# Kernel tuning notes

Hardware: AMD Instinct MI355X
Metric: run time of the kernel (lower is better)

## Reference

```python
import jax, jax.numpy as jnp
import numpy as np

N = 100000        # nodes
E = 3200000       # edges (avg degree 32)
IN_F = 128
OUT_F = 64
ALPHA = 0.2       # LeakyReLU negative slope
EPS = 1e-5        # LayerNorm eps


def setup_inputs() -> dict:
    key = jax.random.key(0)
    k = jax.random.split(key, 5)
    x = jax.random.normal(k[0], (N, IN_F), jnp.float32)
    edge = jax.random.randint(k[1], (2, E), 0, N, dtype=jnp.int32)
    # kaiming-normal inits as in the torch module
    W = jax.random.normal(k[2], (OUT_F, IN_F), jnp.float32) * np.float32(np.sqrt(2.0 / IN_F))
    b = jnp.zeros((OUT_F,), jnp.float32)
    a = jax.random.normal(k[3], (2 * OUT_F,), jnp.float32) * np.float32(np.sqrt(2.0 / (2 * OUT_F)))
    gamma = jnp.ones((OUT_F,), jnp.float32)
    beta = jnp.zeros((OUT_F,), jnp.float32)
    return {"x": x, "edge": edge, "W": W, "b": b, "a": a, "gamma": gamma, "beta": beta}


def reference(x, edge, W, b, a, gamma, beta):
    # h = Linear(in->out)
    h = x @ W.T + b                                   # [N, OUT_F]
    src, dst = edge[0], edge[1]
    # edge score a · cat(h[src], h[dst]) == (h @ a_l)[src] + (h @ a_r)[dst]
    sl = h @ a[:OUT_F]                                # [N]
    sr = h @ a[OUT_F:]                                # [N]
    score = sl[src] + sr[dst]                         # [E]
    lrelu = jnp.where(score > 0, score, ALPHA * score)
    edge_e = jnp.exp(-lrelu)                          # [E] (dropout=0 / eval)
    # sparse spmm: h_prime[i] = sum_{e: src_e==i} edge_e * h[dst_e]
    msg = edge_e[:, None] * h[dst]                    # [E, OUT_F]
    h_prime = jax.ops.segment_sum(msg, src, num_segments=N)  # [N, OUT_F]
    # LayerNorm over feature dim (biased variance, as torch)
    mu = jnp.mean(h_prime, axis=-1, keepdims=True)
    var = jnp.mean(jnp.square(h_prime - mu), axis=-1, keepdims=True)
    h_norm = (h_prime - mu) * jax.lax.rsqrt(var + EPS) * gamma + beta
    # concat=True -> ELU
    return jax.nn.elu(h_norm)
```

## Files before the change

kernel.cpp:

```cpp
#include <hip/hip_runtime.h>
#include <hip/hip_fp16.h>
#include <cstdint>
#include <cstddef>

#define INF_  128
#define OUTF  64
#define ALPHA 0.2f
#define LN_EPS 1e-5f

#define PBLK2 256
#define BT2   512
#define TILE  8192
#define NP2   784
#define NPS   1024
#define PCAP2 48
#define LOC2  128
#define CSRCAP 4608

typedef __attribute__((ext_vector_type(8))) _Float16 half8;
typedef __attribute__((ext_vector_type(4))) float    f32x4;

__global__ __launch_bounds__(256) void gemm_kernel(
    const float* __restrict__ x, const float* __restrict__ W,
    const float* __restrict__ b, const float* __restrict__ a,
    __half* __restrict__ hh, float* __restrict__ sl, float* __restrict__ sr, int n)
{
    __shared__ half8 wfrag_lds[16][64];

    const int tid  = threadIdx.x;
    const int lane = tid & 63;
    const int wv   = tid >> 6;
    const int col  = lane & 15;
    const int quad = lane >> 4;

    for (int idx = tid; idx < 1024; idx += 256) {
        const int l  = idx & 63, ct = idx >> 6;
        const int c  = ct >> 2,  t  = ct & 3;
        const int row = 4 * (l & 15) + t;
        const int k0  = 32 * c + 8 * (l >> 4);
        const float4 f0 = ((const float4*)W)[row * 32 + (k0 >> 2)];
        const float4 f1 = ((const float4*)W)[row * 32 + (k0 >> 2) + 1];
        half8 h;
        h[0] = (_Float16)f0.x; h[1] = (_Float16)f0.y;
        h[2] = (_Float16)f0.z; h[3] = (_Float16)f0.w;
        h[4] = (_Float16)f1.x; h[5] = (_Float16)f1.y;
        h[6] = (_Float16)f1.z; h[7] = (_Float16)f1.w;
        wfrag_lds[ct][l] = h;
    }
    __syncthreads();

    half8 bf[4][4];
    #pragma unroll
    for (int c = 0; c < 4; c++)
        #pragma unroll
        for (int t = 0; t < 4; t++)
            bf[c][t] = wfrag_lds[c * 4 + t][lane];

    const float4 b4  = ((const float4*)b)[col];
    const float4 al4 = ((const float4*)a)[col];
    const float4 ar4 = ((const float4*)a)[16 + col];

    const int ntile  = (n + 15) >> 4;
    const int wgid   = blockIdx.x * 4 + wv;
    const int nwaves = gridDim.x * 4;

    for (int tile = wgid; tile < ntile; tile += nwaves) {
        const int node0 = tile << 4;
        const int xr    = min(node0 + col, n - 1);
        const float* xrow = x + (size_t)xr * INF_ + 8 * quad;

        f32x4 acc0 = {0,0,0,0}, acc1 = {0,0,0,0}, acc2 = {0,0,0,0}, acc3 = {0,0,0,0};
        #pragma unroll
        for (int c = 0; c < 4; c++) {
            const float4 f0 = *(const float4*)(xrow + 32 * c);
            const float4 f1 = *(const float4*)(xrow + 32 * c + 4);
            half8 af;
            af[0] = (_Float16)f0.x; af[1] = (_Float16)f0.y;
            af[2] = (_Float16)f0.z; af[3] = (_Float16)f0.w;
            af[4] = (_Float16)f1.x; af[5] = (_Float16)f1.y;
            af[6] = (_Float16)f1.z; af[7] = (_Float16)f1.w;
            acc0 = __builtin_amdgcn_mfma_f32_16x16x32_f16(af, bf[c][0], acc0, 0, 0, 0);
            acc1 = __builtin_amdgcn_mfma_f32_16x16x32_f16(af, bf[c][1], acc1, 0, 0, 0);
            acc2 = __builtin_amdgcn_mfma_f32_16x16x32_f16(af, bf[c][2], acc2, 0, 0, 0);
            acc3 = __builtin_amdgcn_mfma_f32_16x16x32_f16(af, bf[c][3], acc3, 0, 0, 0);
        }

        #pragma unroll
        for (int reg = 0; reg < 4; reg++) {
            const int node = node0 + quad * 4 + reg;
            const float v0 = acc0[reg] + b4.x;
            const float v1 = acc1[reg] + b4.y;
            const float v2 = acc2[reg] + b4.z;
            const float v3 = acc3[reg] + b4.w;
            float p = v0 * al4.x + v1 * al4.y + v2 * al4.z + v3 * al4.w;
            float q = v0 * ar4.x + v1 * ar4.y + v2 * ar4.z + v3 * ar4.w;
            p += __shfl_xor(p, 1); p += __shfl_xor(p, 2);
            p += __shfl_xor(p, 4); p += __shfl_xor(p, 8);
            q += __shfl_xor(q, 1); q += __shfl_xor(q, 2);
            q += __shfl_xor(q, 4); q += __shfl_xor(q, 8);
            if (node < n) {
                ushort4 u;
                u.x = __half_as_ushort(__float2half(v0));
                u.y = __half_as_ushort(__float2half(v1));
                u.z = __half_as_ushort(__float2half(v2));
                u.w = __half_as_ushort(__float2half(v3));
                ((ushort4*)hh)[(size_t)node * 16 + col] = u;
                if (col == 0) { sl[node] = p; sr[node] = q; }
            }
        }
    }
}

__global__ __launch_bounds__(512) void part_scatter(
    const int* __restrict__ src, const int* __restrict__ dst,
    int* __restrict__ pka, int* __restrict__ acnt, int E)
{
    __shared__ int hist[NPS];
    __shared__ int bnd[NPS + 1];
    __shared__ int cur[NPS];
    __shared__ int gbase[NP2];
    __shared__ int buf[TILE];
    __shared__ int csum[16];
    __shared__ int csb[16];

    const int t    = threadIdx.x;
    const int b    = blockIdx.x;
    const int lane = t & 63;
    const int wv   = t >> 6;

    for (int i = t; i < NP2; i += 512) gbase[i] = 0;

    const int chunk = (E + PBLK2 - 1) / PBLK2;
    const int lo = b * chunk;
    const int hi = min(E, lo + chunk);

    for (int tb = lo; tb < hi; tb += TILE) {
        const int tcnt = min(TILE, hi - tb);
        for (int i = t; i < NPS; i += 512) hist[i] = 0;
        __syncthreads();

        int pp[16], pay[16];
        #pragma unroll
        for (int k = 0; k < 16; k++) {
            const int e = tb + t + k * 512;
            pp[k] = -1;
            if (e < hi) {
                const int s = src[e];
                pp[k]  = s >> 7;
                pay[k] = ((s & 127) << 17) | dst[e];
                atomicAdd(&hist[pp[k]], 1);
            }
        }
        __syncthreads();

        int vA = hist[wv * 64 + lane];
        int vB = hist[(wv + 8) * 64 + lane];
        int sA = vA, sB = vB;
        #pragma unroll
        for (int d = 1; d < 64; d <<= 1) {
            const int uA = __shfl(sA, lane - d);
            const int uB = __shfl(sB, lane - d);
            if (lane >= d) { sA += uA; sB += uB; }
        }
        if (lane == 63) { csum[wv] = sA; csum[wv + 8] = sB; }
        __syncthreads();
        if (t == 0) {
            int r = 0;
            #pragma unroll
            for (int c2 = 0; c2 < 16; c2++) { csb[c2] = r; r += csum[c2]; }
            bnd[NPS] = r;
        }
        __syncthreads();
        {
            const int eA = csb[wv] + sA - vA;
            const int eB = csb[wv + 8] + sB - vB;
            bnd[wv * 64 + lane]       = eA;
            bnd[(wv + 8) * 64 + lane] = eB;
            cur[wv * 64 + lane]       = eA;
            cur[(wv + 8) * 64 + lane] = eB;
        }
        __syncthreads();

        #pragma unroll
        for (int k = 0; k < 16; k++) {
            if (pp[k] >= 0) {
                const int r = atomicAdd(&cur[pp[k]], 1);
                buf[r] = pay[k];
            }
        }
        __syncthreads();

        for (int idx = t; idx < tcnt; idx += 512) {
            int p = 0;
            #pragma unroll
            for (int step = 512; step >= 1; step >>= 1)
                if (bnd[p + step] <= idx) p += step;
            const int off = gbase[p] + (idx - bnd[p]);
            if (off < PCAP2)
                pka[(size_t)((p << 8) | b) * PCAP2 + off] = buf[idx];
        }
        __syncthreads();

        for (int p = t; p < NP2; p += 512) gbase[p] += bnd[p + 1] - bnd[p];
        __syncthreads();
    }

    for (int p = t; p < NP2; p += 512)
        acnt[p * PBLK2 + b] = min(gbase[p], PCAP2);
}

__global__ __launch_bounds__(512) void gat_fused(
    const int* __restrict__ pka, const int* __restrict__ acnt,
    const float* __restrict__ sl, const float* __restrict__ sr,
    const __half* __restrict__ hh,
    const float* __restrict__ gamma, const float* __restrict__ beta,
    float* __restrict__ out, int n)
{
    __shared__ int    ldst[CSRCAP];
    __shared__ __half lwgt[CSRCAP];
    __shared__ int    alen[PBLK2];
    __shared__ float  lsl[LOC2];
    __shared__ int    lhist[LOC2];
    __shared__ int    lbase[LOC2 + 1];
    __shared__ int    cur2[LOC2];
    __shared__ int    wtot_;

    const int B     = blockIdx.x;
    const int t     = threadIdx.x;
    const int lane  = t & 63;
    const int wv    = t >> 6;
    const int fgrp  = lane & 15;
    const int equad = lane >> 4;

    for (int i = t; i < PBLK2; i += 512) alen[i] = acnt[B * PBLK2 + i];
    if (t < LOC2) {
        lhist[t] = 0;
        const int g = (B << 7) + t;
        lsl[t] = (g < n) ? sl[g] : 0.f;
    }
    __syncthreads();

    const int4* slab4 = (const int4*)(pka + (size_t)(B << 8) * PCAP2);

    for (int i = t; i < 3072; i += 512) {
        const int j0  = i << 2;
        const int seg = j0 / PCAP2;
        const int off = j0 - seg * PCAP2;
        const int m   = alen[seg] - off;
        if (m > 0) {
            const int4 v4 = slab4[i];
            atomicAdd(&lhist[(v4.x >> 17) & 127], 1);
            if (m > 1) atomicAdd(&lhist[(v4.y >> 17) & 127], 1);
            if (m > 2) atomicAdd(&lhist[(v4.z >> 17) & 127], 1);
            if (m > 3) atomicAdd(&lhist[(v4.w >> 17) & 127], 1);
        }
    }
    __syncthreads();

    int sv = 0, vv = 0;
    if (t < 128) {
        vv = lhist[t]; sv = vv;
        #pragma unroll
        for (int d = 1; d < 64; d <<= 1) {
            const int u = __shfl(sv, lane - d);
            if (lane >= d) sv += u;
        }
        if (t == 63) wtot_ = sv;
    }
    __syncthreads();
    if (t < 128) {
        const int base = (t >= 64) ? wtot_ : 0;
        const int eb = base + sv - vv;
        lbase[t] = eb; cur2[t] = eb;
        if (t == 127) lbase[128] = base + sv;
    }
    __syncthreads();

    for (int i = t; i < 3072; i += 512) {
        const int j0  = i << 2;
        const int seg = j0 / PCAP2;
        const int off = j0 - seg * PCAP2;
        const int m   = alen[seg] - off;
        if (m > 0) {
            const int4 v4 = slab4[i];
            #pragma unroll
            for (int c = 0; c < 4; c++) {
                if (c < m) {
                    const int v = (c == 0) ? v4.x : (c == 1) ? v4.y : (c == 2) ? v4.z : v4.w;
                    const int s = (v >> 17) & 127;
                    const int d = v & 0x1FFFF;
                    const float sc = lsl[s] + sr[d];
                    const float lr = sc > 0.f ? sc : ALPHA * sc;
                    const int p = atomicAdd(&cur2[s], 1);
                    if (p < CSRCAP) {
                        ldst[p] = d;
                        lwgt[p] = __float2half(__expf(-lr));
                    }
                }
            }
        }
    }
    __syncthreads();

    const float4 gm4 = ((const float4*)gamma)[fgrp];
    const float4 bt4 = ((const float4*)beta)[fgrp];

    for (int k = wv; k < LOC2; k += 8) {
        const int node = (B << 7) + k;
        const int nb   = min(lbase[k], CSRCAP);
        const int ne   = min(lbase[k + 1], CSRCAP);
        const int len  = ne - nb;

        float4 acc = make_float4(0.f, 0.f, 0.f, 0.f);

        const int e0 = equad, e1 = 4 + equad;
        int dA = 0, dB = 0; float wA = 0.f, wB = 0.f;
        if (e0 < len) { dA = ldst[nb + e0]; wA = __half2float(lwgt[nb + e0]); }
        if (e1 < len) { dB = ldst[nb + e1]; wB = __half2float(lwgt[nb + e1]); }
        uint2 uA = ((const uint2*)hh)[(size_t)dA * 16 + fgrp];
        uint2 uB = ((const uint2*)hh)[(size_t)dB * 16 + fgrp];

        for (int tt = 0; tt < len; tt += 8) {
            uint2 nA = make_uint2(0u, 0u), nB = make_uint2(0u, 0u);
            float nwA = 0.f, nwB = 0.f;
            if (tt + 8 < len) {
                const int f0 = tt + 8 + equad, f1 = tt + 12 + equad;
                int xA = 0, xB = 0;
                if (f0 < len) { xA = ldst[nb + f0]; nwA = __half2float(lwgt[nb + f0]); }
                if (f1 < len) { xB = ldst[nb + f1]; nwB = __half2float(lwgt[nb + f1]); }
                nA = ((const uint2*)hh)[(size_t)xA * 16 + fgrp];
                nB = ((const uint2*)hh)[(size_t)xB * 16 + fgrp];
            }
            const float2 fA0 = __half22float2(*(const __half2*)&uA.x);
            const float2 fA1 = __half22float2(*(const __half2*)&uA.y);
            const float2 fB0 = __half22float2(*(const __half2*)&uB.x);
            const float2 fB1 = __half22float2(*(const __half2*)&uB.y);
            acc.x = fmaf(wA, fA0.x, acc.x); acc.y = fmaf(wA, fA0.y, acc.y);
            acc.z = fmaf(wA, fA1.x, acc.z); acc.w = fmaf(wA, fA1.y, acc.w);
            acc.x = fmaf(wB, fB0.x, acc.x); acc.y = fmaf(wB, fB0.y, acc.y);
            acc.z = fmaf(wB, fB1.x, acc.z); acc.w = fmaf(wB, fB1.y, acc.w);
            uA = nA; uB = nB; wA = nwA; wB = nwB;
        }

        acc.x += __shfl_xor(acc.x, 16); acc.x += __shfl_xor(acc.x, 32);
        acc.y += __shfl_xor(acc.y, 16); acc.y += __shfl_xor(acc.y, 32);
        acc.z += __shfl_xor(acc.z, 16); acc.z += __shfl_xor(acc.z, 32);
        acc.w += __shfl_xor(acc.w, 16); acc.w += __shfl_xor(acc.w, 32);

        float s1 = acc.x + acc.y + acc.z + acc.w;
        float s2 = acc.x * acc.x + acc.y * acc.y + acc.z * acc.z + acc.w * acc.w;
        #pragma unroll
        for (int dd = 1; dd < 16; dd <<= 1) {
            s1 += __shfl_xor(s1, dd);
            s2 += __shfl_xor(s2, dd);
        }
        const float mu  = s1 * (1.f / 64.f);
        const float var = fmaxf(s2 * (1.f / 64.f) - mu * mu, 0.f);
        const float rs  = rsqrtf(var + LN_EPS);

        float4 y;
        y.x = (acc.x - mu) * rs * gm4.x + bt4.x;
        y.y = (acc.y - mu) * rs * gm4.y + bt4.y;
        y.z = (acc.z - mu) * rs * gm4.z + bt4.z;
        y.w = (acc.w - mu) * rs * gm4.w + bt4.w;
        y.x = y.x > 0.f ? y.x : __expf(y.x) - 1.f;
        y.y = y.y > 0.f ? y.y : __expf(y.y) - 1.f;
        y.z = y.z > 0.f ? y.z : __expf(y.z) - 1.f;
        y.w = y.w > 0.f ? y.w : __expf(y.w) - 1.f;
        if (node < n && equad == 0)
            ((float4*)out)[(size_t)node * 16 + fgrp] = y;
    }
}

extern "C" void kernel_launch(void* const* d_in, const int* in_sizes, int n_in,
                              void* d_out, int out_size, void* d_ws, size_t ws_size,
                              hipStream_t stream)
{
    const float* x     = (const float*)d_in[0];
    const int*   edge  = (const int*)  d_in[1];
    const float* W     = (const float*)d_in[2];
    const float* b     = (const float*)d_in[3];
    const float* a     = (const float*)d_in[4];
    const float* gamma = (const float*)d_in[5];
    const float* beta  = (const float*)d_in[6];
    float* out = (float*)d_out;

    const int n = in_sizes[0] / INF_;
    const int E = in_sizes[1] / 2;
    const int* src = edge;
    const int* dst = edge + E;
    const int npart = (n + LOC2 - 1) >> 7;

    char* ws = (char*)d_ws;
    size_t offb = 0;
    auto alloc = [&](size_t bytes) -> void* {
        void* p = ws + offb;
        offb = (offb + bytes + 255) & ~(size_t)255;
        return p;
    };
    __half* hh   = (__half*)alloc((size_t)n * OUTF * 2);
    float*  sl   = (float*) alloc((size_t)n * 4);
    float*  sr   = (float*) alloc((size_t)n * 4);
    int*    acnt = (int*)   alloc((size_t)NP2 * PBLK2 * 4);
    int*    pka  = (int*)   alloc((size_t)NP2 * PBLK2 * PCAP2 * 4);

    hipLaunchKernelGGL(part_scatter, dim3(PBLK2), dim3(BT2), 0, stream, src, dst, pka, acnt, E);
    hipLaunchKernelGGL(gemm_kernel,  dim3(1024),  dim3(256), 0, stream, x, W, b, a, hh, sl, sr, n);
    hipLaunchKernelGGL(gat_fused,    dim3(npart), dim3(512), 0, stream, pka, acnt, sl, sr, hh, gamma, beta, out, n);
}
```

Before: 250.9 us.

## Replace capped per-block partition slabs with exact count-scan-scatter compact layout

Adds a count pass and a single-block scan so the partition scatter writes edges into an exactly sized, contiguous per-partition array instead of fixed-capacity padded slabs. The consumer kernel then reads a dense range, computes edge weights once in registers, and places them using ranks taken from the histogram atomics, which removes the second slab pass and the cur2 atomics. The scatter also stores the partition id byte-wise so it no longer needs a binary search per element. The cost is an extra read of src, a serial single-block scan over a 784x512 matrix, and two more launches.

After: 392.7 us. 56.5% more time.

```diff
diff --git a/kernel.cpp b/kernel.cpp
--- a/kernel.cpp
+++ b/kernel.cpp
@@ -8,14 +8,13 @@
 #define ALPHA 0.2f
 #define LN_EPS 1e-5f
 
-#define PBLK2 256
-#define BT2   512
-#define TILE  8192
+#define PBLK  512
 #define NP2   784
 #define NPS   1024
-#define PCAP2 48
+#define TILE  6656
 #define LOC2  128
 #define CSRCAP 4608
+#define MAXK  9
 
 typedef __attribute__((ext_vector_type(8))) _Float16 half8;
 typedef __attribute__((ext_vector_type(4))) float    f32x4;
@@ -111,15 +110,69 @@
     }
 }
 
+__global__ __launch_bounds__(512) void count_kernel(
+    const int* __restrict__ src, int* __restrict__ M, int E)
+{
+    __shared__ int hist[NPS];
+    const int t = threadIdx.x;
+    const int b = blockIdx.x;
+    for (int i = t; i < NPS; i += 512) hist[i] = 0;
+    __syncthreads();
+    const int chunk = (E + PBLK - 1) / PBLK;
+    const int lo = b * chunk;
+    const int hi = min(E, lo + chunk);
+    for (int e = lo + t; e < hi; e += 512)
+        atomicAdd(&hist[src[e] >> 7], 1);
+    __syncthreads();
+    for (int p = t; p < NP2; p += 512)
+        M[(size_t)p * PBLK + b] = hist[p];
+}
+
+__global__ __launch_bounds__(1024) void scan_kernel(
+    int* __restrict__ M, int* __restrict__ pbase)
+{
+    __shared__ int part[1024];
+    const int t = threadIdx.x;
+    int tot = 0;
+    if (t < NP2) {
+        const int4* row = (const int4*)(M + (size_t)t * PBLK);
+        for (int i = 0; i < PBLK / 4; i++) {
+            const int4 v = row[i];
+            tot += v.x + v.y + v.z + v.w;
+        }
+    }
+    part[t] = tot;
+    __syncthreads();
+    for (int d = 1; d < 1024; d <<= 1) {
+        const int v = (t >= d) ? part[t - d] : 0;
+        __syncthreads();
+        part[t] += v;
+        __syncthreads();
+    }
+    const int excl = part[t] - tot;
+    if (t < NP2) {
+        pbase[t] = excl;
+        if (t == NP2 - 1) pbase[NP2] = part[t];
+        int run = excl;
+        int* row = M + (size_t)t * PBLK;
+        for (int i = 0; i < PBLK; i++) {
+            const int c = row[i];
+            row[i] = run;
+            run += c;
+        }
+    }
+}
+
 __global__ __launch_bounds__(512) void part_scatter(
     const int* __restrict__ src, const int* __restrict__ dst,
-    int* __restrict__ pka, int* __restrict__ acnt, int E)
+    const int* __restrict__ M, int* __restrict__ pk, int E)
 {
     __shared__ int hist[NPS];
     __shared__ int bnd[NPS + 1];
     __shared__ int cur[NPS];
     __shared__ int gbase[NP2];
     __shared__ int buf[TILE];
+    __shared__ unsigned char pbuf[TILE];
     __shared__ int csum[16];
     __shared__ int csb[16];
 
@@ -128,9 +181,9 @@
     const int lane = t & 63;
     const int wv   = t >> 6;
 
-    for (int i = t; i < NP2; i += 512) gbase[i] = 0;
-
-    const int chunk = (E + PBLK2 - 1) / PBLK2;
+    for (int p = t; p < NP2; p += 512) gbase[p] = M[(size_t)p * PBLK + b];
+
+    const int chunk = (E + PBLK - 1) / PBLK;
     const int lo = b * chunk;
     const int hi = min(E, lo + chunk);
 
@@ -139,9 +192,9 @@
         for (int i = t; i < NPS; i += 512) hist[i] = 0;
         __syncthreads();
 
-        int pp[16], pay[16];
-        #pragma unroll
-        for (int k = 0; k < 16; k++) {
+        int pp[13], pay[13];
+        #pragma unroll
+        for (int k = 0; k < 13; k++) {
             const int e = tb + t + k * 512;
             pp[k] = -1;
             if (e < hi) {
@@ -182,35 +235,30 @@
         __syncthreads();
 
         #pragma unroll
-        for (int k = 0; k < 16; k++) {
+        for (int k = 0; k < 13; k++) {
             if (pp[k] >= 0) {
                 const int r = atomicAdd(&cur[pp[k]], 1);
-                buf[r] = pay[k];
+                buf[r]  = pay[k];
+                pbuf[r] = (unsigned char)(pp[k] & 255);
             }
         }
         __syncthreads();
 
+        const int c1 = bnd[256], c2_ = bnd[512], c3 = bnd[768];
         for (int idx = t; idx < tcnt; idx += 512) {
-            int p = 0;
-            #pragma unroll
-            for (int step = 512; step >= 1; step >>= 1)
-                if (bnd[p + step] <= idx) p += step;
-            const int off = gbase[p] + (idx - bnd[p]);
-            if (off < PCAP2)
-                pka[(size_t)((p << 8) | b) * PCAP2 + off] = buf[idx];
+            const int phi = (idx >= c1) + (idx >= c2_) + (idx >= c3);
+            const int p   = (phi << 8) | (int)pbuf[idx];
+            pk[gbase[p] + (idx - bnd[p])] = buf[idx];
         }
         __syncthreads();
 
         for (int p = t; p < NP2; p += 512) gbase[p] += bnd[p + 1] - bnd[p];
         __syncthreads();
     }
-
-    for (int p = t; p < NP2; p += 512)
-        acnt[p * PBLK2 + b] = min(gbase[p], PCAP2);
 }
 
 __global__ __launch_bounds__(512) void gat_fused(
-    const int* __restrict__ pka, const int* __restrict__ acnt,
+    const int* __restrict__ pk, const int* __restrict__ pbase,
     const float* __restrict__ sl, const float* __restrict__ sr,
     const __half* __restrict__ hh,
     const float* __restrict__ gamma, const float* __restrict__ beta,
@@ -218,11 +266,9 @@
 {
     __shared__ int    ldst[CSRCAP];
     __shared__ __half lwgt[CSRCAP];
-    __shared__ int    alen[PBLK2];
     __shared__ float  lsl[LOC2];
     __shared__ int    lhist[LOC2];
     __shared__ int    lbase[LOC2 + 1];
-    __shared__ int    cur2[LOC2];
     __shared__ int    wtot_;
 
     const int B     = blockIdx.x;
@@ -232,27 +278,29 @@
     const int fgrp  = lane & 15;
     const int equad = lane >> 4;
 
-    for (int i = t; i < PBLK2; i += 512) alen[i] = acnt[B * PBLK2 + i];
     if (t < LOC2) {
         lhist[t] = 0;
         const int g = (B << 7) + t;
         lsl[t] = (g < n) ? sl[g] : 0.f;
     }
-    __syncthreads();
-
-    const int4* slab4 = (const int4*)(pka + (size_t)(B << 8) * PCAP2);
-
-    for (int i = t; i < 3072; i += 512) {
-        const int j0  = i << 2;
-        const int seg = j0 / PCAP2;
-        const int off = j0 - seg * PCAP2;
-        const int m   = alen[seg] - off;
-        if (m > 0) {
-            const int4 v4 = slab4[i];
-            atomicAdd(&lhist[(v4.x >> 17) & 127], 1);
-            if (m > 1) atomicAdd(&lhist[(v4.y >> 17) & 127], 1);
-            if (m > 2) atomicAdd(&lhist[(v4.z >> 17) & 127], 1);
-            if (m > 3) atomicAdd(&lhist[(v4.w >> 17) & 127], 1);
+    const int p0  = pbase[B];
+    const int cnt = min(pbase[B + 1] - p0, CSRCAP);
+    __syncthreads();
+
+    const int myn = (cnt > t) ? (cnt - t + 511) >> 9 : 0;
+    int   pkr[MAXK];
+    float wf[MAXK];
+    int   rk[MAXK];
+    #pragma unroll
+    for (int k = 0; k < MAXK; k++) {
+        if (k < myn) {
+            const int v = pk[p0 + t + (k << 9)];
+            pkr[k] = v;
+            const int s = (v >> 17) & 127;
+            rk[k] = atomicAdd(&lhist[s], 1);
+            const float sc = lsl[s] + sr[v & 0x1FFFF];
+            const float lr = sc > 0.f ? sc : ALPHA * sc;
+            wf[k] = __expf(-lr);
         }
     }
     __syncthreads();
@@ -270,34 +318,19 @@
     __syncthreads();
     if (t < 128) {
         const int base = (t >= 64) ? wtot_ : 0;
-        const int eb = base + sv - vv;
-        lbase[t] = eb; cur2[t] = eb;
+        lbase[t] = base + sv - vv;
         if (t == 127) lbase[128] = base + sv;
     }
     __syncthreads();
 
-    for (int i = t; i < 3072; i += 512) {
-        const int j0  = i << 2;
-        const int seg = j0 / PCAP2;
-        const int off = j0 - seg * PCAP2;
-        const int m   = alen[seg] - off;
-        if (m > 0) {
-            const int4 v4 = slab4[i];
-            #pragma unroll
-            for (int c = 0; c < 4; c++) {
-                if (c < m) {
-                    const int v = (c == 0) ? v4.x : (c == 1) ? v4.y : (c == 2) ? v4.z : v4.w;
-                    const int s = (v >> 17) & 127;
-                    const int d = v & 0x1FFFF;
-                    const float sc = lsl[s] + sr[d];
-                    const float lr = sc > 0.f ? sc : ALPHA * sc;
-                    const int p = atomicAdd(&cur2[s], 1);
-                    if (p < CSRCAP) {
-                        ldst[p] = d;
-                        lwgt[p] = __float2half(__expf(-lr));
-                    }
-                }
-            }
+    #pragma unroll
+    for (int k = 0; k < MAXK; k++) {
+        if (k < myn) {
+            const int v = pkr[k];
+            const int s = (v >> 17) & 127;
+            const int p = lbase[s] + rk[k];
+            ldst[p] = v & 0x1FFFF;
+            lwgt[p] = __float2half(wf[k]);
         }
     }
     __syncthreads();
@@ -307,9 +340,8 @@
 
     for (int k = wv; k < LOC2; k += 8) {
         const int node = (B << 7) + k;
-        const int nb   = min(lbase[k], CSRCAP);
-        const int ne   = min(lbase[k + 1], CSRCAP);
-        const int len  = ne - nb;
+        const int nb   = lbase[k];
+        const int len  = lbase[k + 1] - nb;
 
         float4 acc = make_float4(0.f, 0.f, 0.f, 0.f);
 
@@ -398,13 +430,16 @@
         offb = (offb + bytes + 255) & ~(size_t)255;
         return p;
     };
-    __half* hh   = (__half*)alloc((size_t)n * OUTF * 2);
-    float*  sl   = (float*) alloc((size_t)n * 4);
-    float*  sr   = (float*) alloc((size_t)n * 4);
-    int*    acnt = (int*)   alloc((size_t)NP2 * PBLK2 * 4);
-    int*    pka  = (int*)   alloc((size_t)NP2 * PBLK2 * PCAP2 * 4);
-
-    hipLaunchKernelGGL(part_scatter, dim3(PBLK2), dim3(BT2), 0, stream, src, dst, pka, acnt, E);
-    hipLaunchKernelGGL(gemm_kernel,  dim3(1024),  dim3(256), 0, stream, x, W, b, a, hh, sl, sr, n);
-    hipLaunchKernelGGL(gat_fused,    dim3(npart), dim3(512), 0, stream, pka, acnt, sl, sr, hh, gamma, beta, out, n);
-}
+    __half* hh    = (__half*)alloc((size_t)n * OUTF * 2);
+    float*  sl    = (float*) alloc((size_t)n * 4);
+    float*  sr    = (float*) alloc((size_t)n * 4);
+    int*    M     = (int*)   alloc((size_t)NP2 * PBLK * 4);
+    int*    pbase = (int*)   alloc((size_t)(NP2 + 1) * 4);
+    int*    pk    = (int*)   alloc((size_t)E * 4);
+
+    hipLaunchKernelGGL(count_kernel, dim3(PBLK),  dim3(512),  0, stream, src, M, E);
+    hipLaunchKernelGGL(scan_kernel,  dim3(1),     dim3(1024), 0, stream, M, pbase);
+    hipLaunchKernelGGL(gemm_kernel,  dim3(1024),  dim3(256),  0, stream, x, W, b, a, hh, sl, sr, n);
+    hipLaunchKernelGGL(part_scatter, dim3(PBLK),  dim3(512),  0, stream, src, dst, M, pk, E);
+    hipLaunchKernelGGL(gat_fused,    dim3(npart), dim3(512),  0, stream, pk, pbase, sl, sr, hh, gamma, beta, out, n);
+}
```
